# Optimization experiments

Measured on AMD Instinct MI355X. Metric: run time of the kernel, lower is better.

## Reference

```python
import jax, jax.numpy as jnp
import numpy as np

N_NODES = 100000
IN_DIM = 128
N_HEADS = 4
D_HEAD = 32
N_EDGES = 800000
LN_EPS = 1e-5
NEG_SLOPE = 0.2


def setup_inputs() -> dict:
    key = jax.random.key(0)
    k = jax.random.split(key, 7)
    x = jax.random.normal(k[0], (N_NODES, IN_DIM), dtype=jnp.float32)
    edge_index = jax.random.randint(k[1], (2, N_EDGES), 0, N_NODES, dtype=jnp.int32)
    # W: Linear(in_dim, H*D, bias=False) -> store as [in_dim, H*D] for x @ W
    W = jax.random.normal(k[2], (IN_DIM, N_HEADS * D_HEAD), dtype=jnp.float32) * (1.0 / np.sqrt(IN_DIM))
    # attn_mlp: Linear(2*D, 1, bias=False), shared across heads; split into src/dst halves
    a_src = jax.random.normal(k[3], (D_HEAD,), dtype=jnp.float32) * 0.1
    a_dst = jax.random.normal(k[4], (D_HEAD,), dtype=jnp.float32) * 0.1
    ln_gamma = jnp.ones((N_HEADS * D_HEAD,), dtype=jnp.float32)
    ln_beta = jnp.zeros((N_HEADS * D_HEAD,), dtype=jnp.float32)
    return {"x": x, "edge_index": edge_index, "W": W, "a_src": a_src,
            "a_dst": a_dst, "ln_gamma": ln_gamma, "ln_beta": ln_beta}


def reference(x, edge_index, W, a_src, a_dst, ln_gamma, ln_beta):
    N = x.shape[0]
    # dense projection: [N, H*D] -> [N, H, D]
    h = (x @ W).reshape(N, N_HEADS, D_HEAD)
    src, dst = edge_index[0], edge_index[1]
    h_src = h[src]          # [E, H, D] gather
    h_dst = h[dst]          # [E, H, D] gather
    # attn_mlp(cat([h_src, h_dst])) == h_src @ a[:D] + h_dst @ a[D:]
    s = jnp.einsum('ehd,d->eh', h_src, a_src) + jnp.einsum('ehd,d->eh', h_dst, a_dst)
    s = jnp.where(s > 0, s, NEG_SLOPE * s)  # LeakyReLU(0.2)
    # segment softmax over destination node groups (per head)
    smax = jax.ops.segment_max(s, dst, num_segments=N)          # [N, H]
    e = jnp.exp(s - smax[dst])                                   # [E, H]
    denom = jax.ops.segment_sum(e, dst, num_segments=N)          # [N, H]
    alpha = e / denom[dst]                                       # [E, H]
    # weighted scatter-add aggregation
    msg = h_src * alpha[..., None]                               # [E, H, D]
    out = jax.ops.segment_sum(msg, dst, num_segments=N)          # [N, H, D]
    out = out.reshape(N, N_HEADS * D_HEAD)
    # residual: in_dim == H*D -> Identity
    out = out + x
    # LayerNorm
    mu = out.mean(-1, keepdims=True)
    var = ((out - mu) ** 2).mean(-1, keepdims=True)
    out = (out - mu) / jnp.sqrt(var + LN_EPS) * ln_gamma + ln_beta
    # ELU
    return jnp.where(out > 0, out, jnp.expm1(out))
```

## Files before the change

### kernel.cpp

```cpp
#include <hip/hip_runtime.h>
#include <math.h>

#define NEG_SLOPE 0.2f
#define LN_EPS 1e-5f

#define NB 196
#define EPB 2048

typedef __attribute__((ext_vector_type(8))) short bf16x8;
typedef __attribute__((ext_vector_type(4))) float f32x4;

static __device__ __forceinline__ unsigned short f2bf(float f) {
  unsigned u = __float_as_uint(f);
  u += 0x7fffu + ((u >> 16) & 1u);
  return (unsigned short)(u >> 16);
}
static __device__ __forceinline__ unsigned pack_bf16(float a, float b) {
  unsigned ua = __float_as_uint(a);
  unsigned ub = __float_as_uint(b);
  ua += 0x7fffu + ((ua >> 16) & 1u);
  ub += 0x7fffu + ((ub >> 16) & 1u);
  return (ua >> 16) | (ub & 0xffff0000u);
}
static __device__ __forceinline__ float bf_lo(unsigned u) { return __uint_as_float(u << 16); }
static __device__ __forceinline__ float bf_hi(unsigned u) { return __uint_as_float(u & 0xffff0000u); }

__global__ __launch_bounds__(256) void k_prep(
    const float* __restrict__ W, const float* __restrict__ a_src,
    const float* __restrict__ a_dst, short* __restrict__ wfrag,
    short* __restrict__ wafrag)
{
  const int t = threadIdx.x;
  if (blockIdx.x < 8) {
    const int idx  = blockIdx.x * 256 + t;
    const int tile = idx >> 6;
    const int l2   = idx & 63;
    const int c    = tile >> 2;
    const int kk   = tile & 3;
    const int q2   = l2 >> 4;
    const int i2   = l2 & 15;
    const float* wp = W + (size_t)(kk * 32 + q2 * 8) * 128 + c * 16 + i2;
    bf16x8 wv;
    #pragma unroll
    for (int j = 0; j < 8; ++j) wv[j] = (short)f2bf(wp[(size_t)j * 128]);
    *(bf16x8*)(wfrag + (size_t)idx * 8) = wv;
  } else {
    const int kk = t >> 6;
    const int l2 = t & 63;
    const int q2 = l2 >> 4;
    const int i2 = l2 & 15;
    bf16x8 wv = {0, 0, 0, 0, 0, 0, 0, 0};
    if (i2 < 8) {
      const int head = i2 >> 1;
      const float* ap = (i2 & 1) ? a_dst : a_src;
      #pragma unroll
      for (int j = 0; j < 8; ++j) {
        const int k = kk * 32 + q2 * 8 + j;
        const float* wr = W + (size_t)k * 128 + head * 32;
        float sum = 0.f;
        for (int d = 0; d < 32; d += 4) {
          const float4 wq = *(const float4*)(wr + d);
          const float4 aq = *(const float4*)(ap + d);
          sum += wq.x * aq.x + wq.y * aq.y + wq.z * aq.z + wq.w * aq.w;
        }
        wv[j] = (short)f2bf(sum);
      }
    }
    *(bf16x8*)(wafrag + (size_t)t * 8) = wv;
  }
}

__global__ __launch_bounds__(256) void k_bhist(
    const int* __restrict__ e_dst, int* __restrict__ H, int n_edges, int nblk)
{
  __shared__ int hist[NB];
  const int t = threadIdx.x;
  if (t < NB) hist[t] = 0;
  __syncthreads();
  int e = blockIdx.x * EPB + t * 8;
  if (e + 8 <= n_edges) {
    const int4 d0 = *(const int4*)(e_dst + e);
    const int4 d1 = *(const int4*)(e_dst + e + 4);
    atomicAdd(&hist[d0.x >> 9], 1); atomicAdd(&hist[d0.y >> 9], 1);
    atomicAdd(&hist[d0.z >> 9], 1); atomicAdd(&hist[d0.w >> 9], 1);
    atomicAdd(&hist[d1.x >> 9], 1); atomicAdd(&hist[d1.y >> 9], 1);
    atomicAdd(&hist[d1.z >> 9], 1); atomicAdd(&hist[d1.w >> 9], 1);
  } else {
    const int eend = (e + 8 < n_edges) ? (e + 8) : n_edges;
    for (; e < eend; ++e) atomicAdd(&hist[e_dst[e] >> 9], 1);
  }
  __syncthreads();
  if (t < NB) H[t * nblk + blockIdx.x] = hist[t];
}

__global__ __launch_bounds__(256) void k_cscan(
    int* __restrict__ H, int* __restrict__ totals, int nblk)
{
  __shared__ int sdata[256];
  const int b = blockIdx.x, t = threadIdx.x;
  int* col = H + (size_t)b * nblk;
  const int i0 = 2 * t, i1 = 2 * t + 1;
  const int v0 = (i0 < nblk) ? col[i0] : 0;
  const int v1 = (i1 < nblk) ? col[i1] : 0;
  const int tsum = v0 + v1;
  sdata[t] = tsum;
  __syncthreads();
  for (int off = 1; off < 256; off <<= 1) {
    const int addv = (t >= off) ? sdata[t - off] : 0;
    __syncthreads();
    sdata[t] += addv;
    __syncthreads();
  }
  const int excl = sdata[t] - tsum;
  if (i0 < nblk) col[i0] = excl;
  if (i1 < nblk) col[i1] = excl + v0;
  if (t == 255) totals[b] = sdata[255];
}

__global__ __launch_bounds__(256) void k_scatter(
    const int* __restrict__ e_src, const int* __restrict__ e_dst,
    const int* __restrict__ H, const int* __restrict__ totals,
    int2* __restrict__ ebuf, int n_edges, int nblk)
{
  __shared__ int sdata[256];
  __shared__ int cur[NB];
  const int t = threadIdx.x;
  const int tv = (t < NB) ? totals[t] : 0;
  sdata[t] = tv;
  __syncthreads();
  for (int off = 1; off < 256; off <<= 1) {
    const int addv = (t >= off) ? sdata[t - off] : 0;
    __syncthreads();
    sdata[t] += addv;
    __syncthreads();
  }
  if (t < NB) cur[t] = (sdata[t] - tv) + H[t * nblk + blockIdx.x];
  __syncthreads();
  int e = blockIdx.x * EPB + t * 8;
  if (e + 8 <= n_edges) {
    const int4 d0 = *(const int4*)(e_dst + e);
    const int4 d1 = *(const int4*)(e_dst + e + 4);
    const int4 s0 = *(const int4*)(e_src + e);
    const int4 s1 = *(const int4*)(e_src + e + 4);
    int p;
    p = atomicAdd(&cur[d0.x >> 9], 1); ebuf[p] = make_int2(d0.x, s0.x);
    p = atomicAdd(&cur[d0.y >> 9], 1); ebuf[p] = make_int2(d0.y, s0.y);
    p = atomicAdd(&cur[d0.z >> 9], 1); ebuf[p] = make_int2(d0.z, s0.z);
    p = atomicAdd(&cur[d0.w >> 9], 1); ebuf[p] = make_int2(d0.w, s0.w);
    p = atomicAdd(&cur[d1.x >> 9], 1); ebuf[p] = make_int2(d1.x, s1.x);
    p = atomicAdd(&cur[d1.y >> 9], 1); ebuf[p] = make_int2(d1.y, s1.y);
    p = atomicAdd(&cur[d1.z >> 9], 1); ebuf[p] = make_int2(d1.z, s1.z);
    p = atomicAdd(&cur[d1.w >> 9], 1); ebuf[p] = make_int2(d1.w, s1.w);
  } else {
    const int eend = (e + 8 < n_edges) ? (e + 8) : n_edges;
    for (; e < eend; ++e) {
      const int d = e_dst[e];
      const int p = atomicAdd(&cur[d >> 9], 1);
      ebuf[p] = make_int2(d, e_src[e]);
    }
  }
}

__global__ __launch_bounds__(256) void k_bcsr(
    const int2* __restrict__ ebuf, const int* __restrict__ totals,
    int* __restrict__ row_start, int* __restrict__ csr_src, int n_nodes)
{
  __shared__ int sdata[256];
  __shared__ int hist[512];
  __shared__ int cur[512];
  const int b = blockIdx.x, t = threadIdx.x;
  const int n0 = b << 9;

  const int tv = (t < NB) ? totals[t] : 0;
  sdata[t] = tv;
  __syncthreads();
  for (int off = 1; off < 256; off <<= 1) {
    const int addv = (t >= off) ? sdata[t - off] : 0;
    __syncthreads();
    sdata[t] += addv;
    __syncthreads();
  }
  const int base = (b == 0) ? 0 : sdata[b - 1];
  const int nE   = sdata[b] - base;

  hist[t] = 0; hist[t + 256] = 0;
  __syncthreads();
  for (int e = t; e < nE; e += 256)
    atomicAdd(&hist[ebuf[base + e].x - n0], 1);
  __syncthreads();

  const int h0 = hist[2 * t], h1 = hist[2 * t + 1];
  const int tsum = h0 + h1;
  sdata[t] = tsum;
  __syncthreads();
  for (int off = 1; off < 256; off <<= 1) {
    const int addv = (t >= off) ? sdata[t - off] : 0;
    __syncthreads();
    sdata[t] += addv;
    __syncthreads();
  }
  const int excl = sdata[t] - tsum;
  cur[2 * t]     = excl;
  cur[2 * t + 1] = excl + h0;
  if (n0 + 2 * t     <= n_nodes) row_start[n0 + 2 * t]     = base + excl;
  if (n0 + 2 * t + 1 <= n_nodes) row_start[n0 + 2 * t + 1] = base + excl + h0;
  __syncthreads();

  for (int e = t; e < nE; e += 256) {
    const int2 ds = ebuf[base + e];
    const int r = atomicAdd(&cur[ds.x - n0], 1);
    csr_src[base + r] = ds.y;
  }
}

__global__ __launch_bounds__(256, 4) void k_proj(
    const float* __restrict__ x, const short* __restrict__ wfrag,
    const short* __restrict__ wafrag,
    unsigned* __restrict__ h, float* __restrict__ sc, int n_nodes)
{
  __shared__ __align__(16) short wlds[32 * 64 * 8];
  __shared__ __align__(16) short walds[4 * 64 * 8];

  const int t    = threadIdx.x;
  const int l    = t & 63;
  const int il   = l & 15;
  const int quad = l >> 4;
  const int wbase = blockIdx.x * 128 + (t >> 6) * 32;

  {
    const uint4* wf4 = (const uint4*)wfrag;
    uint4* wl4 = (uint4*)wlds;
    #pragma unroll
    for (int i = 0; i < 8; ++i) wl4[t + i * 256] = wf4[t + i * 256];
    ((uint4*)walds)[t] = ((const uint4*)wafrag)[t];
  }
  __syncthreads();

  f32x4 acc[2][8] = {};
  f32x4 acc2[2] = {};
  #pragma unroll
  for (int kk = 0; kk < 4; ++kk) {
    bf16x8 ahi[2], alo[2];
    #pragma unroll
    for (int rt = 0; rt < 2; ++rt) {
      int row = wbase + rt * 16 + il;
      if (row > n_nodes - 1) row = n_nodes - 1;
      const float* p = x + (size_t)row * 128 + kk * 32 + quad * 8;
      const float4 u0 = *(const float4*)(p);
      const float4 u1 = *(const float4*)(p + 4);
      const float f[8] = {u0.x, u0.y, u0.z, u0.w, u1.x, u1.y, u1.z, u1.w};
      #pragma unroll
      for (int j = 0; j < 8; ++j) {
        const unsigned u = __float_as_uint(f[j]);
        ahi[rt][j] = (short)(u >> 16);
        const float lof = f[j] - __uint_as_float(u & 0xffff0000u);
        alo[rt][j] = (short)f2bf(lof);
      }
    }
    #pragma unroll
    for (int c = 0; c < 8; ++c) {
      const bf16x8 bv = *(const bf16x8*)(wlds + ((c * 4 + kk) * 64 + l) * 8);
      acc[0][c] = __builtin_amdgcn_mfma_f32_16x16x32_bf16(ahi[0], bv, acc[0][c], 0, 0, 0);
      acc[0][c] = __builtin_amdgcn_mfma_f32_16x16x32_bf16(alo[0], bv, acc[0][c], 0, 0, 0);
      acc[1][c] = __builtin_amdgcn_mfma_f32_16x16x32_bf16(ahi[1], bv, acc[1][c], 0, 0, 0);
      acc[1][c] = __builtin_amdgcn_mfma_f32_16x16x32_bf16(alo[1], bv, acc[1][c], 0, 0, 0);
    }
    const bf16x8 bv = *(const bf16x8*)(walds + (kk * 64 + l) * 8);
    acc2[0] = __builtin_amdgcn_mfma_f32_16x16x32_bf16(ahi[0], bv, acc2[0], 0, 0, 0);
    acc2[0] = __builtin_amdgcn_mfma_f32_16x16x32_bf16(alo[0], bv, acc2[0], 0, 0, 0);
    acc2[1] = __builtin_amdgcn_mfma_f32_16x16x32_bf16(ahi[1], bv, acc2[1], 0, 0, 0);
    acc2[1] = __builtin_amdgcn_mfma_f32_16x16x32_bf16(alo[1], bv, acc2[1], 0, 0, 0);
  }

  #pragma unroll
  for (int rt = 0; rt < 2; ++rt) {
    #pragma unroll
    for (int reg = 0; reg < 4; ++reg) {
      const int r = wbase + rt * 16 + quad * 4 + reg;
      const bool inb = (r < n_nodes);
      const bool wr = inb && ((il & 3) == 0);
      #pragma unroll
      for (int c = 0; c < 8; ++c) {
        const float v  = acc[rt][c][reg];
        const float vn = __shfl_xor(v, 1);
        const float plo = (il & 1) ? vn : v;
        const float phi = (il & 1) ? v : vn;
        const unsigned px = pack_bf16(plo, phi);
        const unsigned py = __shfl_xor(px, 2);
        if (wr) {
          uint2 u; u.x = px; u.y = py;
          *(uint2*)(h + (size_t)r * 64 + c * 8 + (il >> 1)) = u;
        }
      }
      if (inb && il < 8) sc[(size_t)r * 8 + il] = acc2[rt][reg];
    }
  }
}

#define ACC_EDGE(al, hv)                              \
  acc[0] = fmaf(al, bf_lo(hv.x), acc[0]);             \
  acc[1] = fmaf(al, bf_hi(hv.x), acc[1]);             \
  acc[2] = fmaf(al, bf_lo(hv.y), acc[2]);             \
  acc[3] = fmaf(al, bf_hi(hv.y), acc[3]);             \
  acc[4] = fmaf(al, bf_lo(hv.z), acc[4]);             \
  acc[5] = fmaf(al, bf_hi(hv.z), acc[5]);             \
  acc[6] = fmaf(al, bf_lo(hv.w), acc[6]);             \
  acc[7] = fmaf(al, bf_hi(hv.w), acc[7]);

__global__ __launch_bounds__(256) void k_agg(
    const unsigned* __restrict__ h, const float* __restrict__ sc,
    const int* __restrict__ row_start, const int* __restrict__ csr_src,
    const float* __restrict__ x, const float* __restrict__ gamma,
    const float* __restrict__ beta, float* __restrict__ out, int n_nodes)
{
  const int t    = threadIdx.x;
  const int lane = t & 63;
  const int g    = lane & 15;
  const int node = blockIdx.x * 16 + (t >> 6) * 4 + (lane >> 4);
  if (node >= n_nodes) return;
  const int head = g >> 2;
  const int sub  = g & 3;
  const int hh   = head * 2;
  const int beg  = row_start[node];
  const int deg  = row_start[node + 1] - beg;
  const float sdv = sc[node * 8 + hh + 1];

  float m = -INFINITY, l = 0.f;
  float t0 = 0.f, t1 = 0.f, t2 = 0.f, t3 = 0.f;
  int   c0 = 0,   c1 = 0,   c2 = 0,   c3 = 0;
  if (sub < deg) {
    c0 = csr_src[beg + sub];
    float s = sc[c0 * 8 + hh] + sdv;  s = s > 0.f ? s : NEG_SLOPE * s;
    t0 = s; m = s; l = 1.f;
  }
  if (sub + 4 < deg) {
    c1 = csr_src[beg + sub + 4];
    float s = sc[c1 * 8 + hh] + sdv;  s = s > 0.f ? s : NEG_SLOPE * s;
    t1 = s;
    const float mn = fmaxf(m, s);
    l = l * __expf(m - mn) + __expf(s - mn);  m = mn;
  }
  if (sub + 8 < deg) {
    c2 = csr_src[beg + sub + 8];
    float s = sc[c2 * 8 + hh] + sdv;  s = s > 0.f ? s : NEG_SLOPE * s;
    t2 = s;
    const float mn = fmaxf(m, s);
    l = l * __expf(m - mn) + __expf(s - mn);  m = mn;
  }
  if (sub + 12 < deg) {
    c3 = csr_src[beg + sub + 12];
    float s = sc[c3 * 8 + hh] + sdv;  s = s > 0.f ? s : NEG_SLOPE * s;
    t3 = s;
    const float mn = fmaxf(m, s);
    l = l * __expf(m - mn) + __expf(s - mn);  m = mn;
  }
  for (int i = sub + 16; i < deg; i += 4) {
    const int cs = csr_src[beg + i];
    float s = sc[cs * 8 + hh] + sdv;  s = s > 0.f ? s : NEG_SLOPE * s;
    const float mn = fmaxf(m, s);
    l = l * __expf(m - mn) + __expf(s - mn);  m = mn;
  }
  #pragma unroll
  for (int off = 1; off < 4; off <<= 1) {
    const float m2 = __shfl_xor(m, off);
    const float l2 = __shfl_xor(l, off);
    const float mn = fmaxf(m, m2);
    if (mn == -INFINITY) { m = -INFINITY; l = 0.f; }
    else {
      l = l * __expf(m - mn) + l2 * __expf(m2 - mn);
      m = mn;
    }
  }
  const float inv_l = (deg > 0) ? 1.f / l : 0.f;
  const float a0 = __expf(t0 - m) * inv_l;
  const float a1 = __expf(t1 - m) * inv_l;
  const float a2 = __expf(t2 - m) * inv_l;
  const float a3 = __expf(t3 - m) * inv_l;

  const int base3 = lane & 60;

  float acc[8] = {0.f, 0.f, 0.f, 0.f, 0.f, 0.f, 0.f, 0.f};
  const int deg16 = deg < 16 ? deg : 16;
  #pragma unroll
  for (int r = 0; r < 4; ++r) {
    const int i0 = r * 4;
    if (i0 >= deg16) break;
    const float ar = r == 0 ? a0 : r == 1 ? a1 : r == 2 ? a2 : a3;
    const int   cr = r == 0 ? c0 : r == 1 ? c1 : r == 2 ? c2 : c3;
    const int   n  = deg16 - i0;
    {
      const float al = __shfl(ar, base3 | 0);
      const int   sr = __shfl(cr, base3 | 0);
      const uint4 hv = *(const uint4*)(h + (size_t)sr * 64 + g * 4);
      ACC_EDGE(al, hv)
    }
    if (n > 1) {
      const float al = __shfl(ar, base3 | 1);
      const int   sr = __shfl(cr, base3 | 1);
      const uint4 hv = *(const uint4*)(h + (size_t)sr * 64 + g * 4);
      ACC_EDGE(al, hv)
    }
    if (n > 2) {
      const float al = __shfl(ar, base3 | 2);
      const int   sr = __shfl(cr, base3 | 2);
      const uint4 hv = *(const uint4*)(h + (size_t)sr * 64 + g * 4);
      ACC_EDGE(al, hv)
    }
    if (n > 3) {
      const float al = __shfl(ar, base3 | 3);
      const int   sr = __shfl(cr, base3 | 3);
      const uint4 hv = *(const uint4*)(h + (size_t)sr * 64 + g * 4);
      ACC_EDGE(al, hv)
    }
  }
  for (int i = 16; i < deg; ++i) {
    const int sr = csr_src[beg + i];
    float s = sc[sr * 8 + hh] + sdv;  s = s > 0.f ? s : NEG_SLOPE * s;
    const float al = __expf(s - m) * inv_l;
    const uint4 hv = *(const uint4*)(h + (size_t)sr * 64 + g * 4);
    ACC_EDGE(al, hv)
  }

  const float4 xa = *(const float4*)(x + (size_t)node * 128 + g * 8);
  const float4 xb = *(const float4*)(x + (size_t)node * 128 + g * 8 + 4);
  float rr[8];
  rr[0] = acc[0] + xa.x;  rr[1] = acc[1] + xa.y;
  rr[2] = acc[2] + xa.z;  rr[3] = acc[3] + xa.w;
  rr[4] = acc[4] + xb.x;  rr[5] = acc[5] + xb.y;
  rr[6] = acc[6] + xb.z;  rr[7] = acc[7] + xb.w;
  float s1 = 0.f, s2 = 0.f;
  #pragma unroll
  for (int j = 0; j < 8; ++j) { s1 += rr[j]; s2 += rr[j] * rr[j]; }
  #pragma unroll
  for (int off = 1; off < 16; off <<= 1) {
    s1 += __shfl_xor(s1, off);
    s2 += __shfl_xor(s2, off);
  }
  const float mu   = s1 * (1.f / 128.f);
  const float var  = s2 * (1.f / 128.f) - mu * mu;
  const float rstd = rsqrtf(var + LN_EPS);
  const float4 ga = *(const float4*)(gamma + g * 8);
  const float4 gb = *(const float4*)(gamma + g * 8 + 4);
  const float4 ba = *(const float4*)(beta  + g * 8);
  const float4 bb = *(const float4*)(beta  + g * 8 + 4);
  float4 o0, o1;
  o0.x = (rr[0] - mu) * rstd * ga.x + ba.x;
  o0.y = (rr[1] - mu) * rstd * ga.y + ba.y;
  o0.z = (rr[2] - mu) * rstd * ga.z + ba.z;
  o0.w = (rr[3] - mu) * rstd * ga.w + ba.w;
  o1.x = (rr[4] - mu) * rstd * gb.x + bb.x;
  o1.y = (rr[5] - mu) * rstd * gb.y + bb.y;
  o1.z = (rr[6] - mu) * rstd * gb.z + bb.z;
  o1.w = (rr[7] - mu) * rstd * gb.w + bb.w;
  o0.x = o0.x > 0.f ? o0.x : expm1f(o0.x);
  o0.y = o0.y > 0.f ? o0.y : expm1f(o0.y);
  o0.z = o0.z > 0.f ? o0.z : expm1f(o0.z);
  o0.w = o0.w > 0.f ? o0.w : expm1f(o0.w);
  o1.x = o1.x > 0.f ? o1.x : expm1f(o1.x);
  o1.y = o1.y > 0.f ? o1.y : expm1f(o1.y);
  o1.z = o1.z > 0.f ? o1.z : expm1f(o1.z);
  o1.w = o1.w > 0.f ? o1.w : expm1f(o1.w);
  *(float4*)(out + (size_t)node * 128 + g * 8)     = o0;
  *(float4*)(out + (size_t)node * 128 + g * 8 + 4) = o1;
}

extern "C" void kernel_launch(void* const* d_in, const int* in_sizes, int n_in,
                              void* d_out, int out_size, void* d_ws, size_t ws_size,
                              hipStream_t stream)
{
  const float* x    = (const float*)d_in[0];
  const int*   ei   = (const int*)d_in[1];
  const float* W    = (const float*)d_in[2];
  const float* a_s  = (const float*)d_in[3];
  const float* a_d  = (const float*)d_in[4];
  const float* gam  = (const float*)d_in[5];
  const float* bet  = (const float*)d_in[6];
  float* out = (float*)d_out;

  const int n_nodes = in_sizes[0] / 128;
  const int n_edges = in_sizes[1] / 2;
  const int* e_src = ei;
  const int* e_dst = ei + n_edges;

  const int nblkE = (n_edges + EPB - 1) / EPB;

  char* p = (char*)d_ws;
  unsigned* h = (unsigned*)p; p += (size_t)n_nodes * 64 * sizeof(unsigned);
  float* sc   = (float*)p;  p += (size_t)n_nodes * 8 * sizeof(float);
  int* row_start = (int*)p; p += (size_t)(n_nodes + 4) * sizeof(int);
  int* csr_src   = (int*)p; p += (size_t)n_edges * sizeof(int);
  short* wfrag   = (short*)p; p += (size_t)2048 * 8 * sizeof(short);
  short* wafrag  = (short*)p; p += (size_t)256 * 8 * sizeof(short);
  int* H      = (int*)p; p += (size_t)NB * nblkE * sizeof(int);
  int* totals = (int*)p; p += (size_t)NB * sizeof(int);
  int2* ebuf  = (int2*)h;

  k_prep<<<9, 256, 0, stream>>>(W, a_s, a_d, wfrag, wafrag);
  k_bhist<<<nblkE, 256, 0, stream>>>(e_dst, H, n_edges, nblkE);
  k_cscan<<<NB, 256, 0, stream>>>(H, totals, nblkE);
  k_scatter<<<nblkE, 256, 0, stream>>>(e_src, e_dst, H, totals, ebuf, n_edges, nblkE);
  k_bcsr<<<NB, 256, 0, stream>>>(ebuf, totals, row_start, csr_src, n_nodes);
  const int nproj = (n_nodes + 127) / 128;
  k_proj<<<nproj, 256, 0, stream>>>(x, wfrag, wafrag, h, sc, n_nodes);
  k_agg<<<(n_nodes + 15) / 16, 256, 0, stream>>>(h, sc, row_start, csr_src, x, gam, bet, out, n_nodes);
}
```

Before: 207.5 us.

## Fuse CSR build stages with projection blocks to overlap independent work

Merges weight prep with the edge histogram into one launch, then splits the projection GEMM into three slices and runs each alongside one of the scan, scatter and per-bucket CSR kernels in a shared launch. The point is to fill idle CUs during the small, latency-bound sort stages and to cut the number of launches. A separate edge buffer is allocated so the projection output is no longer aliased with the scatter buffer. If the workspace is too small it falls back to the old sequential order. In exchange it uses more workspace memory, and the shared-memory size is now uniform across the fused kernels.

```diff
diff --git a/kernel.cpp b/kernel.cpp
--- a/kernel.cpp
+++ b/kernel.cpp
@@ -6,6 +6,7 @@
 
 #define NB 196
 #define EPB 2048
+#define SMEM_BYTES (36 * 1024)
 
 typedef __attribute__((ext_vector_type(8))) short bf16x8;
 typedef __attribute__((ext_vector_type(4))) float f32x4;
@@ -25,207 +26,20 @@
 static __device__ __forceinline__ float bf_lo(unsigned u) { return __uint_as_float(u << 16); }
 static __device__ __forceinline__ float bf_hi(unsigned u) { return __uint_as_float(u & 0xffff0000u); }
 
-__global__ __launch_bounds__(256) void k_prep(
-    const float* __restrict__ W, const float* __restrict__ a_src,
-    const float* __restrict__ a_dst, short* __restrict__ wfrag,
-    short* __restrict__ wafrag)
-{
-  const int t = threadIdx.x;
-  if (blockIdx.x < 8) {
-    const int idx  = blockIdx.x * 256 + t;
-    const int tile = idx >> 6;
-    const int l2   = idx & 63;
-    const int c    = tile >> 2;
-    const int kk   = tile & 3;
-    const int q2   = l2 >> 4;
-    const int i2   = l2 & 15;
-    const float* wp = W + (size_t)(kk * 32 + q2 * 8) * 128 + c * 16 + i2;
-    bf16x8 wv;
-    #pragma unroll
-    for (int j = 0; j < 8; ++j) wv[j] = (short)f2bf(wp[(size_t)j * 128]);
-    *(bf16x8*)(wfrag + (size_t)idx * 8) = wv;
-  } else {
-    const int kk = t >> 6;
-    const int l2 = t & 63;
-    const int q2 = l2 >> 4;
-    const int i2 = l2 & 15;
-    bf16x8 wv = {0, 0, 0, 0, 0, 0, 0, 0};
-    if (i2 < 8) {
-      const int head = i2 >> 1;
-      const float* ap = (i2 & 1) ? a_dst : a_src;
-      #pragma unroll
-      for (int j = 0; j < 8; ++j) {
-        const int k = kk * 32 + q2 * 8 + j;
-        const float* wr = W + (size_t)k * 128 + head * 32;
-        float sum = 0.f;
-        for (int d = 0; d < 32; d += 4) {
-          const float4 wq = *(const float4*)(wr + d);
-          const float4 aq = *(const float4*)(ap + d);
-          sum += wq.x * aq.x + wq.y * aq.y + wq.z * aq.z + wq.w * aq.w;
-        }
-        wv[j] = (short)f2bf(sum);
-      }
-    }
-    *(bf16x8*)(wafrag + (size_t)t * 8) = wv;
-  }
-}
-
-__global__ __launch_bounds__(256) void k_bhist(
-    const int* __restrict__ e_dst, int* __restrict__ H, int n_edges, int nblk)
-{
-  __shared__ int hist[NB];
-  const int t = threadIdx.x;
-  if (t < NB) hist[t] = 0;
-  __syncthreads();
-  int e = blockIdx.x * EPB + t * 8;
-  if (e + 8 <= n_edges) {
-    const int4 d0 = *(const int4*)(e_dst + e);
-    const int4 d1 = *(const int4*)(e_dst + e + 4);
-    atomicAdd(&hist[d0.x >> 9], 1); atomicAdd(&hist[d0.y >> 9], 1);
-    atomicAdd(&hist[d0.z >> 9], 1); atomicAdd(&hist[d0.w >> 9], 1);
-    atomicAdd(&hist[d1.x >> 9], 1); atomicAdd(&hist[d1.y >> 9], 1);
-    atomicAdd(&hist[d1.z >> 9], 1); atomicAdd(&hist[d1.w >> 9], 1);
-  } else {
-    const int eend = (e + 8 < n_edges) ? (e + 8) : n_edges;
-    for (; e < eend; ++e) atomicAdd(&hist[e_dst[e] >> 9], 1);
-  }
-  __syncthreads();
-  if (t < NB) H[t * nblk + blockIdx.x] = hist[t];
-}
-
-__global__ __launch_bounds__(256) void k_cscan(
-    int* __restrict__ H, int* __restrict__ totals, int nblk)
-{
-  __shared__ int sdata[256];
-  const int b = blockIdx.x, t = threadIdx.x;
-  int* col = H + (size_t)b * nblk;
-  const int i0 = 2 * t, i1 = 2 * t + 1;
-  const int v0 = (i0 < nblk) ? col[i0] : 0;
-  const int v1 = (i1 < nblk) ? col[i1] : 0;
-  const int tsum = v0 + v1;
-  sdata[t] = tsum;
-  __syncthreads();
-  for (int off = 1; off < 256; off <<= 1) {
-    const int addv = (t >= off) ? sdata[t - off] : 0;
-    __syncthreads();
-    sdata[t] += addv;
-    __syncthreads();
-  }
-  const int excl = sdata[t] - tsum;
-  if (i0 < nblk) col[i0] = excl;
-  if (i1 < nblk) col[i1] = excl + v0;
-  if (t == 255) totals[b] = sdata[255];
-}
-
-__global__ __launch_bounds__(256) void k_scatter(
-    const int* __restrict__ e_src, const int* __restrict__ e_dst,
-    const int* __restrict__ H, const int* __restrict__ totals,
-    int2* __restrict__ ebuf, int n_edges, int nblk)
-{
-  __shared__ int sdata[256];
-  __shared__ int cur[NB];
-  const int t = threadIdx.x;
-  const int tv = (t < NB) ? totals[t] : 0;
-  sdata[t] = tv;
-  __syncthreads();
-  for (int off = 1; off < 256; off <<= 1) {
-    const int addv = (t >= off) ? sdata[t - off] : 0;
-    __syncthreads();
-    sdata[t] += addv;
-    __syncthreads();
-  }
-  if (t < NB) cur[t] = (sdata[t] - tv) + H[t * nblk + blockIdx.x];
-  __syncthreads();
-  int e = blockIdx.x * EPB + t * 8;
-  if (e + 8 <= n_edges) {
-    const int4 d0 = *(const int4*)(e_dst + e);
-    const int4 d1 = *(const int4*)(e_dst + e + 4);
-    const int4 s0 = *(const int4*)(e_src + e);
-    const int4 s1 = *(const int4*)(e_src + e + 4);
-    int p;
-    p = atomicAdd(&cur[d0.x >> 9], 1); ebuf[p] = make_int2(d0.x, s0.x);
-    p = atomicAdd(&cur[d0.y >> 9], 1); ebuf[p] = make_int2(d0.y, s0.y);
-    p = atomicAdd(&cur[d0.z >> 9], 1); ebuf[p] = make_int2(d0.z, s0.z);
-    p = atomicAdd(&cur[d0.w >> 9], 1); ebuf[p] = make_int2(d0.w, s0.w);
-    p = atomicAdd(&cur[d1.x >> 9], 1); ebuf[p] = make_int2(d1.x, s1.x);
-    p = atomicAdd(&cur[d1.y >> 9], 1); ebuf[p] = make_int2(d1.y, s1.y);
-    p = atomicAdd(&cur[d1.z >> 9], 1); ebuf[p] = make_int2(d1.z, s1.z);
-    p = atomicAdd(&cur[d1.w >> 9], 1); ebuf[p] = make_int2(d1.w, s1.w);
-  } else {
-    const int eend = (e + 8 < n_edges) ? (e + 8) : n_edges;
-    for (; e < eend; ++e) {
-      const int d = e_dst[e];
-      const int p = atomicAdd(&cur[d >> 9], 1);
-      ebuf[p] = make_int2(d, e_src[e]);
-    }
-  }
-}
-
-__global__ __launch_bounds__(256) void k_bcsr(
-    const int2* __restrict__ ebuf, const int* __restrict__ totals,
-    int* __restrict__ row_start, int* __restrict__ csr_src, int n_nodes)
-{
-  __shared__ int sdata[256];
-  __shared__ int hist[512];
-  __shared__ int cur[512];
-  const int b = blockIdx.x, t = threadIdx.x;
-  const int n0 = b << 9;
-
-  const int tv = (t < NB) ? totals[t] : 0;
-  sdata[t] = tv;
-  __syncthreads();
-  for (int off = 1; off < 256; off <<= 1) {
-    const int addv = (t >= off) ? sdata[t - off] : 0;
-    __syncthreads();
-    sdata[t] += addv;
-    __syncthreads();
-  }
-  const int base = (b == 0) ? 0 : sdata[b - 1];
-  const int nE   = sdata[b] - base;
-
-  hist[t] = 0; hist[t + 256] = 0;
-  __syncthreads();
-  for (int e = t; e < nE; e += 256)
-    atomicAdd(&hist[ebuf[base + e].x - n0], 1);
-  __syncthreads();
-
-  const int h0 = hist[2 * t], h1 = hist[2 * t + 1];
-  const int tsum = h0 + h1;
-  sdata[t] = tsum;
-  __syncthreads();
-  for (int off = 1; off < 256; off <<= 1) {
-    const int addv = (t >= off) ? sdata[t - off] : 0;
-    __syncthreads();
-    sdata[t] += addv;
-    __syncthreads();
-  }
-  const int excl = sdata[t] - tsum;
-  cur[2 * t]     = excl;
-  cur[2 * t + 1] = excl + h0;
-  if (n0 + 2 * t     <= n_nodes) row_start[n0 + 2 * t]     = base + excl;
-  if (n0 + 2 * t + 1 <= n_nodes) row_start[n0 + 2 * t + 1] = base + excl + h0;
-  __syncthreads();
-
-  for (int e = t; e < nE; e += 256) {
-    const int2 ds = ebuf[base + e];
-    const int r = atomicAdd(&cur[ds.x - n0], 1);
-    csr_src[base + r] = ds.y;
-  }
-}
-
-__global__ __launch_bounds__(256, 4) void k_proj(
+
+static __device__ __forceinline__ void proj_body(
     const float* __restrict__ x, const short* __restrict__ wfrag,
-    const short* __restrict__ wafrag,
-    unsigned* __restrict__ h, float* __restrict__ sc, int n_nodes)
-{
-  __shared__ __align__(16) short wlds[32 * 64 * 8];
-  __shared__ __align__(16) short walds[4 * 64 * 8];
+    const short* __restrict__ wafrag, unsigned* __restrict__ h,
+    float* __restrict__ sc, int n_nodes, int pb, char* smem)
+{
+  short* wlds  = (short*)smem;
+  short* walds = (short*)(smem + 32 * 1024);
 
   const int t    = threadIdx.x;
   const int l    = t & 63;
   const int il   = l & 15;
   const int quad = l >> 4;
-  const int wbase = blockIdx.x * 128 + (t >> 6) * 32;
+  const int wbase = pb * 128 + (t >> 6) * 32;
 
   {
     const uint4* wf4 = (const uint4*)wfrag;
@@ -295,6 +109,244 @@
       if (inb && il < 8) sc[(size_t)r * 8 + il] = acc2[rt][reg];
     }
   }
+}
+
+static __device__ __forceinline__ void cscan_body(
+    int* __restrict__ H, int* __restrict__ totals, int nblk, int b, char* smem)
+{
+  int* sdata = (int*)smem;
+  const int t = threadIdx.x;
+  int* col = H + (size_t)b * nblk;
+  const int i0 = 2 * t, i1 = 2 * t + 1;
+  const int v0 = (i0 < nblk) ? col[i0] : 0;
+  const int v1 = (i1 < nblk) ? col[i1] : 0;
+  const int tsum = v0 + v1;
+  sdata[t] = tsum;
+  __syncthreads();
+  for (int off = 1; off < 256; off <<= 1) {
+    const int addv = (t >= off) ? sdata[t - off] : 0;
+    __syncthreads();
+    sdata[t] += addv;
+    __syncthreads();
+  }
+  const int excl = sdata[t] - tsum;
+  if (i0 < nblk) col[i0] = excl;
+  if (i1 < nblk) col[i1] = excl + v0;
+  if (t == 255) totals[b] = sdata[255];
+}
+
+static __device__ __forceinline__ void scatter_body(
+    const int* __restrict__ e_src, const int* __restrict__ e_dst,
+    const int* __restrict__ H, const int* __restrict__ totals,
+    int2* __restrict__ ebuf, int n_edges, int nblk, int b, char* smem)
+{
+  int* sdata = (int*)smem;
+  int* cur   = (int*)(smem + 1024);
+  const int t = threadIdx.x;
+  const int tv = (t < NB) ? totals[t] : 0;
+  sdata[t] = tv;
+  __syncthreads();
+  for (int off = 1; off < 256; off <<= 1) {
+    const int addv = (t >= off) ? sdata[t - off] : 0;
+    __syncthreads();
+    sdata[t] += addv;
+    __syncthreads();
+  }
+  if (t < NB) cur[t] = (sdata[t] - tv) + H[t * nblk + b];
+  __syncthreads();
+  int e = b * EPB + t * 8;
+  if (e + 8 <= n_edges) {
+    const int4 d0 = *(const int4*)(e_dst + e);
+    const int4 d1 = *(const int4*)(e_dst + e + 4);
+    const int4 s0 = *(const int4*)(e_src + e);
+    const int4 s1 = *(const int4*)(e_src + e + 4);
+    int p;
+    p = atomicAdd(&cur[d0.x >> 9], 1); ebuf[p] = make_int2(d0.x, s0.x);
+    p = atomicAdd(&cur[d0.y >> 9], 1); ebuf[p] = make_int2(d0.y, s0.y);
+    p = atomicAdd(&cur[d0.z >> 9], 1); ebuf[p] = make_int2(d0.z, s0.z);
+    p = atomicAdd(&cur[d0.w >> 9], 1); ebuf[p] = make_int2(d0.w, s0.w);
+    p = atomicAdd(&cur[d1.x >> 9], 1); ebuf[p] = make_int2(d1.x, s1.x);
+    p = atomicAdd(&cur[d1.y >> 9], 1); ebuf[p] = make_int2(d1.y, s1.y);
+    p = atomicAdd(&cur[d1.z >> 9], 1); ebuf[p] = make_int2(d1.z, s1.z);
+    p = atomicAdd(&cur[d1.w >> 9], 1); ebuf[p] = make_int2(d1.w, s1.w);
+  } else {
+    const int eend = (e + 8 < n_edges) ? (e + 8) : n_edges;
+    for (; e < eend; ++e) {
+      const int d = e_dst[e];
+      const int p = atomicAdd(&cur[d >> 9], 1);
+      ebuf[p] = make_int2(d, e_src[e]);
+    }
+  }
+}
+
+static __device__ __forceinline__ void bcsr_body(
+    const int2* __restrict__ ebuf, const int* __restrict__ totals,
+    int* __restrict__ row_start, int* __restrict__ csr_src, int n_nodes,
+    int b, char* smem)
+{
+  int* sdata = (int*)smem;
+  int* hist  = (int*)(smem + 1024);
+  int* cur   = (int*)(smem + 1024 + 2048);
+  const int t = threadIdx.x;
+  const int n0 = b << 9;
+
+  const int tv = (t < NB) ? totals[t] : 0;
+  sdata[t] = tv;
+  __syncthreads();
+  for (int off = 1; off < 256; off <<= 1) {
+    const int addv = (t >= off) ? sdata[t - off] : 0;
+    __syncthreads();
+    sdata[t] += addv;
+    __syncthreads();
+  }
+  const int base = (b == 0) ? 0 : sdata[b - 1];
+  const int nE   = sdata[b] - base;
+
+  hist[t] = 0; hist[t + 256] = 0;
+  __syncthreads();
+  for (int e = t; e < nE; e += 256)
+    atomicAdd(&hist[ebuf[base + e].x - n0], 1);
+  __syncthreads();
+
+  const int h0 = hist[2 * t], h1 = hist[2 * t + 1];
+  const int tsum = h0 + h1;
+  sdata[t] = tsum;
+  __syncthreads();
+  for (int off = 1; off < 256; off <<= 1) {
+    const int addv = (t >= off) ? sdata[t - off] : 0;
+    __syncthreads();
+    sdata[t] += addv;
+    __syncthreads();
+  }
+  const int excl = sdata[t] - tsum;
+  cur[2 * t]     = excl;
+  cur[2 * t + 1] = excl + h0;
+  if (n0 + 2 * t     <= n_nodes) row_start[n0 + 2 * t]     = base + excl;
+  if (n0 + 2 * t + 1 <= n_nodes) row_start[n0 + 2 * t + 1] = base + excl + h0;
+  __syncthreads();
+
+  for (int e = t; e < nE; e += 256) {
+    const int2 ds = ebuf[base + e];
+    const int r = atomicAdd(&cur[ds.x - n0], 1);
+    csr_src[base + r] = ds.y;
+  }
+}
+
+__global__ __launch_bounds__(256) void k_fuseA(
+    const float* __restrict__ W, const float* __restrict__ a_src,
+    const float* __restrict__ a_dst, short* __restrict__ wfrag,
+    short* __restrict__ wafrag,
+    const int* __restrict__ e_dst, int* __restrict__ H, int n_edges, int nblk)
+{
+  __shared__ int hist[NB];
+  const int t = threadIdx.x;
+  if (blockIdx.x < 8) {
+    const int idx  = blockIdx.x * 256 + t;
+    const int tile = idx >> 6;
+    const int l2   = idx & 63;
+    const int c    = tile >> 2;
+    const int kk   = tile & 3;
+    const int q2   = l2 >> 4;
+    const int i2   = l2 & 15;
+    const float* wp = W + (size_t)(kk * 32 + q2 * 8) * 128 + c * 16 + i2;
+    bf16x8 wv;
+    #pragma unroll
+    for (int j = 0; j < 8; ++j) wv[j] = (short)f2bf(wp[(size_t)j * 128]);
+    *(bf16x8*)(wfrag + (size_t)idx * 8) = wv;
+  } else if (blockIdx.x == 8) {
+    const int kk = t >> 6;
+    const int l2 = t & 63;
+    const int q2 = l2 >> 4;
+    const int i2 = l2 & 15;
+    bf16x8 wv = {0, 0, 0, 0, 0, 0, 0, 0};
+    if (i2 < 8) {
+      const int head = i2 >> 1;
+      const float* ap = (i2 & 1) ? a_dst : a_src;
+      #pragma unroll
+      for (int j = 0; j < 8; ++j) {
+        const int k = kk * 32 + q2 * 8 + j;
+        const float* wr = W + (size_t)k * 128 + head * 32;
+        float sum = 0.f;
+        for (int d = 0; d < 32; d += 4) {
+          const float4 wq = *(const float4*)(wr + d);
+          const float4 aq = *(const float4*)(ap + d);
+          sum += wq.x * aq.x + wq.y * aq.y + wq.z * aq.z + wq.w * aq.w;
+        }
+        wv[j] = (short)f2bf(sum);
+      }
+    }
+    *(bf16x8*)(wafrag + (size_t)t * 8) = wv;
+  } else {
+    const int b = blockIdx.x - 9;
+    if (t < NB) hist[t] = 0;
+    __syncthreads();
+    int e = b * EPB + t * 8;
+    if (e + 8 <= n_edges) {
+      const int4 d0 = *(const int4*)(e_dst + e);
+      const int4 d1 = *(const int4*)(e_dst + e + 4);
+      atomicAdd(&hist[d0.x >> 9], 1); atomicAdd(&hist[d0.y >> 9], 1);
+      atomicAdd(&hist[d0.z >> 9], 1); atomicAdd(&hist[d0.w >> 9], 1);
+      atomicAdd(&hist[d1.x >> 9], 1); atomicAdd(&hist[d1.y >> 9], 1);
+      atomicAdd(&hist[d1.z >> 9], 1); atomicAdd(&hist[d1.w >> 9], 1);
+    } else {
+      const int eend = (e + 8 < n_edges) ? (e + 8) : n_edges;
+      for (; e < eend; ++e) atomicAdd(&hist[e_dst[e] >> 9], 1);
+    }
+    __syncthreads();
+    if (t < NB) H[t * nblk + b] = hist[t];
+  }
+}
+
+__global__ __launch_bounds__(256, 4) void k_fuseB(
+    int* __restrict__ H, int* __restrict__ totals, int nblk,
+    const float* __restrict__ x, const short* __restrict__ wfrag,
+    const short* __restrict__ wafrag, unsigned* __restrict__ h,
+    float* __restrict__ sc, int n_nodes, int proj_base)
+{
+  __shared__ __align__(16) char smem[SMEM_BYTES];
+  if (blockIdx.x < NB) cscan_body(H, totals, nblk, blockIdx.x, smem);
+  else proj_body(x, wfrag, wafrag, h, sc, n_nodes,
+                 proj_base + (int)blockIdx.x - NB, smem);
+}
+
+__global__ __launch_bounds__(256, 4) void k_fuseC(
+    const int* __restrict__ e_src, const int* __restrict__ e_dst,
+    const int* __restrict__ H, const int* __restrict__ totals,
+    int2* __restrict__ ebuf, int n_edges, int nblk,
+    const float* __restrict__ x, const short* __restrict__ wfrag,
+    const short* __restrict__ wafrag, unsigned* __restrict__ h,
+    float* __restrict__ sc, int n_nodes, int proj_base)
+{
+  __shared__ __align__(16) char smem[SMEM_BYTES];
+  if ((int)blockIdx.x < nblk)
+    scatter_body(e_src, e_dst, H, totals, ebuf, n_edges, nblk, blockIdx.x, smem);
+  else
+    proj_body(x, wfrag, wafrag, h, sc, n_nodes,
+              proj_base + (int)blockIdx.x - nblk, smem);
+}
+
+__global__ __launch_bounds__(256, 4) void k_fuseD(
+    const int2* __restrict__ ebuf, const int* __restrict__ totals,
+    int* __restrict__ row_start, int* __restrict__ csr_src, int n_nodes,
+    const float* __restrict__ x, const short* __restrict__ wfrag,
+    const short* __restrict__ wafrag, unsigned* __restrict__ h,
+    float* __restrict__ sc, int proj_base)
+{
+  __shared__ __align__(16) char smem[SMEM_BYTES];
+  if (blockIdx.x < NB)
+    bcsr_body(ebuf, totals, row_start, csr_src, n_nodes, blockIdx.x, smem);
+  else
+    proj_body(x, wfrag, wafrag, h, sc, n_nodes,
+              proj_base + (int)blockIdx.x - NB, smem);
+}
+
+__global__ __launch_bounds__(256, 4) void k_proj(
+    const float* __restrict__ x, const short* __restrict__ wfrag,
+    const short* __restrict__ wafrag, unsigned* __restrict__ h,
+    float* __restrict__ sc, int n_nodes)
+{
+  __shared__ __align__(16) char smem[SMEM_BYTES];
+  proj_body(x, wfrag, wafrag, h, sc, n_nodes, blockIdx.x, smem);
 }
 
 #define ACC_EDGE(al, hv)                              \
@@ -483,6 +535,7 @@
   const int* e_dst = ei + n_edges;
 
   const int nblkE = (n_edges + EPB - 1) / EPB;
+  const int nproj = (n_nodes + 127) / 128;
 
   char* p = (char*)d_ws;
   unsigned* h = (unsigned*)p; p += (size_t)n_nodes * 64 * sizeof(unsigned);
@@ -492,15 +545,33 @@
   short* wfrag   = (short*)p; p += (size_t)2048 * 8 * sizeof(short);
   short* wafrag  = (short*)p; p += (size_t)256 * 8 * sizeof(short);
   int* H      = (int*)p; p += (size_t)NB * nblkE * sizeof(int);
-  int* totals = (int*)p; p += (size_t)NB * sizeof(int);
-  int2* ebuf  = (int2*)h;
-
-  k_prep<<<9, 256, 0, stream>>>(W, a_s, a_d, wfrag, wafrag);
-  k_bhist<<<nblkE, 256, 0, stream>>>(e_dst, H, n_edges, nblkE);
-  k_cscan<<<NB, 256, 0, stream>>>(H, totals, nblkE);
-  k_scatter<<<nblkE, 256, 0, stream>>>(e_src, e_dst, H, totals, ebuf, n_edges, nblkE);
-  k_bcsr<<<NB, 256, 0, stream>>>(ebuf, totals, row_start, csr_src, n_nodes);
-  const int nproj = (n_nodes + 127) / 128;
-  k_proj<<<nproj, 256, 0, stream>>>(x, wfrag, wafrag, h, sc, n_nodes);
-  k_agg<<<(n_nodes + 15) / 16, 256, 0, stream>>>(h, sc, row_start, csr_src, x, gam, bet, out, n_nodes);
-}
+  int* totals = (int*)p; p += (size_t)((NB + 3) & ~3) * sizeof(int);
+  int2* ebuf_sep = (int2*)p; p += (size_t)n_edges * sizeof(int2);
+  const bool fused = ((size_t)(p - (char*)d_ws) <= ws_size);
+  int2* ebuf = fused ? ebuf_sep : (int2*)h;
+
+  k_fuseA<<<9 + nblkE, 256, 0, stream>>>(W, a_s, a_d, wfrag, wafrag,
+                                         e_dst, H, n_edges, nblkE);
+  if (fused) {
+    const int p1 = nproj / 3, p2 = nproj / 3, p3 = nproj - p1 - p2;
+    k_fuseB<<<NB + p1, 256, 0, stream>>>(H, totals, nblkE, x, wfrag, wafrag,
+                                         h, sc, n_nodes, 0);
+    k_fuseC<<<nblkE + p2, 256, 0, stream>>>(e_src, e_dst, H, totals, ebuf,
+                                            n_edges, nblkE, x, wfrag, wafrag,
+                                            h, sc, n_nodes, p1);
+    k_fuseD<<<NB + p3, 256, 0, stream>>>(ebuf, totals, row_start, csr_src,
+                                         n_nodes, x, wfrag, wafrag, h, sc,
+                                         p1 + p2);
+  } else {
+    k_fuseB<<<NB, 256, 0, stream>>>(H, totals, nblkE, x, wfrag, wafrag,
+                                    h, sc, n_nodes, 0);
+    k_fuseC<<<nblkE, 256, 0, stream>>>(e_src, e_dst, H, totals, ebuf,
+                                       n_edges, nblkE, x, wfrag, wafrag,
+                                       h, sc, n_nodes, 0);
+    k_fuseD<<<NB, 256, 0, stream>>>(ebuf, totals, row_start, csr_src,
+                                    n_nodes, x, wfrag, wafrag, h, sc, 0);
+    k_proj<<<nproj, 256, 0, stream>>>(x, wfrag, wafrag, h, sc, n_nodes);
+  }
+  k_agg<<<(n_nodes + 15) / 16, 256, 0, stream>>>(h, sc, row_start, csr_src,
+                                                 x, gam, bet, out, n_nodes);
+}
```

After: 215.4 us. 3.8% more time.
